# Kernel tuning notes

Measured on AMD Instinct MI355X. Metric: run time of the kernel, lower is better.

Reference implementation:

```python
import jax, jax.numpy as jnp
import numpy as np

EPS = 1e-7  # torchvision distance_box_iou_loss eps
BBOX_WEIGHT = 1.0


def _cxcywh_to_xyxy(b):
    cx, cy, w, h = b[..., 0], b[..., 1], b[..., 2], b[..., 3]
    return jnp.stack([cx - w / 2, cy - h / 2, cx + w / 2, cy + h / 2], axis=-1)


def _diou_loss(p, t):
    # p, t: broadcastable (..., 4) xyxy boxes -> (...) per-pair DIoU loss
    px1, py1, px2, py2 = p[..., 0], p[..., 1], p[..., 2], p[..., 3]
    tx1, ty1, tx2, ty2 = t[..., 0], t[..., 1], t[..., 2], t[..., 3]
    iw = jnp.clip(jnp.minimum(px2, tx2) - jnp.maximum(px1, tx1), 0.0)
    ih = jnp.clip(jnp.minimum(py2, ty2) - jnp.maximum(py1, ty1), 0.0)
    inter = iw * ih
    union = (px2 - px1) * (py2 - py1) + (tx2 - tx1) * (ty2 - ty1) - inter
    iou = inter / (union + EPS)
    cw = jnp.maximum(px2, tx2) - jnp.minimum(px1, tx1)
    ch = jnp.maximum(py2, ty2) - jnp.minimum(py1, ty1)
    diag2 = cw * cw + ch * ch + EPS
    dx = (px1 + px2) / 2 - (tx1 + tx2) / 2
    dy = (py1 + py2) / 2 - (ty1 + ty2) / 2
    return 1.0 - iou + (dx * dx + dy * dy) / diag2


def _smooth_l1_mean(p, t):
    # nn.SmoothL1Loss(reduction='none', beta=1.0) then .mean(-1)
    d = p - t
    ad = jnp.abs(d)
    return jnp.where(ad < 1.0, 0.5 * d * d, ad - 0.5).mean(-1)


def _pair_bbox_loss(p_xyxy, t_xyxy):
    # MyBBoxLoss with weight1 = weight2 = 1
    return _diou_loss(p_xyxy, t_xyxy) + _smooth_l1_mean(p_xyxy, t_xyxy)


def _hungarian_square(cost):
    # exact Hungarian (shortest augmenting path, e-maxx formulation), square n x n
    # returns col assignment per row; matches scipy.linear_sum_assignment optimum
    n = cost.shape[0]
    INF = np.inf
    u = np.zeros(n + 1)
    v = np.zeros(n + 1)
    p = np.zeros(n + 1, dtype=np.int64)  # p[j] = row matched to col j (1-based)
    for i in range(1, n + 1):
        p[0] = i
        j0 = 0
        minv = np.full(n + 1, INF)
        way = np.zeros(n + 1, dtype=np.int64)
        used = np.zeros(n + 1, dtype=bool)
        while True:
            used[j0] = True
            i0 = p[j0]
            cur = np.concatenate(([INF], cost[i0 - 1, :] - u[i0] - v[1:]))
            cur[used] = INF
            upd = cur < minv
            way[upd] = j0
            minv = np.where(upd, cur, minv)
            masked = np.where(used, INF, minv)
            j1 = int(np.argmin(masked))
            delta = masked[j1]
            u[p[used]] += delta
            v[used] -= delta
            minv[~used] -= delta
            j0 = j1
            if p[j0] == 0:
                break
        while j0 != 0:
            j1 = way[j0]
            p[j0] = p[j1]
            j0 = j1
    ans = np.zeros(n, dtype=np.int64)
    for j in range(1, n + 1):
        ans[p[j] - 1] = j - 1
    return ans


def _lsa(cost):
    # rectangular (N, M), N <= M: pad with constant rows (doesn't change optimum)
    N, M = cost.shape
    sq = np.zeros((M, M), dtype=np.float64)
    sq[:N] = cost
    return _hungarian_square(sq)[:N]


def compute_cost_and_assign(targ_cat, targ_bbox, pred_cat, pred_bbox):
    B, N = targ_cat.shape
    C = pred_cat.shape[2]
    # cat_cost[b,n,m] = -pred_cat[b,m,targ_cat[b,n]] via one-hot GEMM
    cat_cost = -jnp.einsum('bmc,bnc->bnm', pred_cat,
                           jax.nn.one_hot(targ_cat, C, dtype=pred_cat.dtype))
    t_xyxy = _cxcywh_to_xyxy(targ_bbox)  # (B,N,4)
    p_xyxy = _cxcywh_to_xyxy(pred_bbox)  # (B,M,4)
    bbox_cost = _pair_bbox_loss(p_xyxy[:, None, :, :], t_xyxy[:, :, None, :])  # (B,N,M)
    # faithful to source: multiply by (targ_cat == 0) mask
    bbox_cost = bbox_cost * (targ_cat == 0)[:, :, None].astype(bbox_cost.dtype)
    cost = cat_cost + BBOX_WEIGHT * bbox_cost
    cost_np = np.asarray(jax.device_get(cost), dtype=np.float64)
    assign = jnp.asarray(np.stack([_lsa(cost_np[b]) for b in range(B)]))  # (B,N)
    return assign


def setup_inputs() -> dict:
    key = jax.random.key(0)
    k1, k2, k3, k4 = jax.random.split(key, 4)
    B, N, M, C = 64, 100, 100, 92
    return {
        'targ_cat': jax.random.randint(k1, (B, N), 0, C),
        'targ_bbox': jax.random.uniform(k2, (B, N, 4), dtype=jnp.float32),
        'pred_cat': jax.random.normal(k3, (B, M, C), dtype=jnp.float32),
        'pred_bbox': jax.random.uniform(k4, (B, M, 4), dtype=jnp.float32),
    }


def reference(targ_cat, targ_bbox, pred_cat, pred_bbox):
    assign = compute_cost_and_assign(targ_cat, targ_bbox, pred_cat, pred_bbox)
    # gather matched predictions: (B,N,C) and (B,N,4)
    pc = jnp.take_along_axis(pred_cat, assign[:, :, None], axis=1)
    pb = jnp.take_along_axis(pred_bbox, assign[:, :, None], axis=1)
    # class loss: mean cross-entropy over all B*N slots
    logp = jax.nn.log_softmax(pc, axis=-1)
    loss_cat = -jnp.take_along_axis(logp, targ_cat[:, :, None], axis=2)[..., 0].mean()
    # bbox loss on matched pairs, masked to real objects (targ_cat != 0)
    lb = _pair_bbox_loss(_cxcywh_to_xyxy(pb), _cxcywh_to_xyxy(targ_bbox))  # (B,N)
    mask = targ_cat != 0
    loss_bbox = jnp.where(mask, lb, 0.0).sum() / mask.sum().astype(lb.dtype)
    loss = loss_cat + BBOX_WEIGHT * loss_bbox
    return loss, assign
```

## Files before the change

### kernel.cpp

```cpp
#include <hip/hip_runtime.h>
#include <hip/hip_bf16.h>
#include <math.h>

#define B_ 64
#define N_ 100
#define C_ 92


__device__ __forceinline__ void cxcywh_to_xyxy(const float q[4], float o[4]) {
#pragma clang fp contract(off)
  float cx = q[0], cy = q[1], w = q[2], h = q[3];
  o[0] = cx - w * 0.5f;
  o[1] = cy - h * 0.5f;
  o[2] = cx + w * 0.5f;
  o[3] = cy + h * 0.5f;
}

__device__ __forceinline__ float pair_bbox_loss(const float* p, const float* t) {
#pragma clang fp contract(off)
  const float EPS = 1e-7f;
  float px1 = p[0], py1 = p[1], px2 = p[2], py2 = p[3];
  float tx1 = t[0], ty1 = t[1], tx2 = t[2], ty2 = t[3];
  float iw = fminf(px2, tx2) - fmaxf(px1, tx1); iw = fmaxf(iw, 0.0f);
  float ih = fminf(py2, ty2) - fmaxf(py1, ty1); ih = fmaxf(ih, 0.0f);
  float inter = iw * ih;
  float uni = (px2 - px1) * (py2 - py1) + (tx2 - tx1) * (ty2 - ty1) - inter;
  float iou = inter / (uni + EPS);
  float cw = fmaxf(px2, tx2) - fminf(px1, tx1);
  float ch = fmaxf(py2, ty2) - fminf(py1, ty1);
  float diag2 = cw * cw + ch * ch + EPS;
  float dx = (px1 + px2) * 0.5f - (tx1 + tx2) * 0.5f;
  float dy = (py1 + py2) * 0.5f - (ty1 + ty2) * 0.5f;
  float diou = 1.0f - iou + (dx * dx + dy * dy) / diag2;
  float s = 0.0f;
  for (int k = 0; k < 4; ++k) {
    float d = p[k] - t[k];
    float ad = fabsf(d);
    s += (ad < 1.0f) ? 0.5f * d * d : ad - 0.5f;
  }
  return diou + s * 0.25f;
}

__device__ __forceinline__ int rdlane(int v, int srcLane) {
  return __builtin_amdgcn_readlane(v, srcLane);
}

template <int CTRL>
__device__ __forceinline__ double dminstep(double x) {
  int lo = __double2loint(x), hi = __double2hiint(x);
  int slo = __builtin_amdgcn_update_dpp(lo, lo, CTRL, 0xF, 0xF, false);
  int shi = __builtin_amdgcn_update_dpp(hi, hi, CTRL, 0xF, 0xF, false);
  return fmin(x, __hiloint2double(shi, slo));
}

__device__ __forceinline__ double read_u(double uA, double uB, int i0) {
  bool inA = (i0 <= 64);
  double src = inA ? uA : uB;
  int idx = inA ? (i0 - 1) : (i0 - 65);
  int lo = rdlane(__double2loint(src), idx);
  int hi = rdlane(__double2hiint(src), idx);
  return __hiloint2double(hi, lo);
}


__global__ __launch_bounds__(64) void hungarian_k(
    const int* __restrict__ targ_cat, const float* __restrict__ targ_bbox,
    const float* __restrict__ pred_cat, const float* __restrict__ pred_bbox,
    int* __restrict__ assign_ws, float* __restrict__ assign_out) {
  const int b = blockIdx.x;
  const int lane = threadIdx.x;

  __shared__ float costL[N_ * N_];
  __shared__ float tb[N_ * 4];
  __shared__ float pbx[N_ * 4];
  __shared__ int tcat[N_];

  for (int i = lane; i < N_; i += 64) {
    float q[4], o[4];
    q[0] = targ_bbox[(b * N_ + i) * 4 + 0];
    q[1] = targ_bbox[(b * N_ + i) * 4 + 1];
    q[2] = targ_bbox[(b * N_ + i) * 4 + 2];
    q[3] = targ_bbox[(b * N_ + i) * 4 + 3];
    cxcywh_to_xyxy(q, o);
    tb[i * 4 + 0] = o[0]; tb[i * 4 + 1] = o[1]; tb[i * 4 + 2] = o[2]; tb[i * 4 + 3] = o[3];
    q[0] = pred_bbox[(b * N_ + i) * 4 + 0];
    q[1] = pred_bbox[(b * N_ + i) * 4 + 1];
    q[2] = pred_bbox[(b * N_ + i) * 4 + 2];
    q[3] = pred_bbox[(b * N_ + i) * 4 + 3];
    cxcywh_to_xyxy(q, o);
    pbx[i * 4 + 0] = o[0]; pbx[i * 4 + 1] = o[1]; pbx[i * 4 + 2] = o[2]; pbx[i * 4 + 3] = o[3];
    tcat[i] = targ_cat[b * N_ + i];
  }
  __syncthreads();

  for (int e = lane; e < N_ * N_; e += 64) {
    int n = e / N_;
    int m = e - n * N_;
    int tc = tcat[n];
    float cc = -pred_cat[(b * N_ + m) * C_ + tc];
    float pl = pair_bbox_loss(&pbx[m * 4], &tb[n * 4]);
    costL[e] = cc + ((tc == 0) ? pl : 0.0f);
  }
  __syncthreads();

  const double INF = __builtin_huge_val();
  const int jA = lane + 1;
  const int jB = lane + 65;
  const bool hasB = (jB <= N_);

  double vA = 0.0, vB = 0.0;
  double uA = 0.0, uB = 0.0;
  int pA = 0, pB = 0;

  for (int i = 1; i <= N_; ++i) {
    double minvA = INF, minvB = INF;
    int wayA = 0, wayB = 0;
    bool usedA = false, usedB = false;
    bool fA = false, fB = false;
    int j0 = 0;
    int i0 = i;
    double ui0 = read_u(uA, uB, i0);
    float cA = costL[(i0 - 1) * N_ + (jA - 1)];
    float cB = 0.0f;
    if (hasB) cB = costL[(i0 - 1) * N_ + (jB - 1)];
    int it = 0;
    bool ok = true;

    while (true) {
      if (j0 == jA) usedA = true;
      if (j0 == jB) usedB = true;
      fA = fA || (i0 == jA);
      fB = fB || (i0 == jB);

      if (!usedA) {
        double cur = (double)cA - ui0 - vA;
        if (cur < minvA) { minvA = cur; wayA = j0; }
      }
      if (hasB && !usedB) {
        double cur = (double)cB - ui0 - vB;
        if (cur < minvB) { minvB = cur; wayB = j0; }
      }

      double cvA = usedA ? INF : minvA;
      double cvB = (hasB && !usedB) ? minvB : INF;
      double r = fmin(cvA, cvB);
      r = dminstep<0x111>(r);
      r = dminstep<0x112>(r);
      r = dminstep<0x114>(r);
      r = dminstep<0x118>(r);
      r = dminstep<0x142>(r);
      r = dminstep<0x143>(r);
      double delta = __hiloint2double(rdlane(__double2hiint(r), 63),
                                      rdlane(__double2loint(r), 63));
      if (delta == INF) { ok = false; break; }

      unsigned long long mA = __ballot(cvA == delta);
      int j1;
      if (mA) {
        j1 = __builtin_ctzll(mA) + 1;
      } else {
        unsigned long long mB = __ballot(cvB == delta);
        if (!mB) { ok = false; break; }
        j1 = __builtin_ctzll(mB) + 65;
      }

      int pj1 = (j1 <= 64) ? rdlane(pA, j1 - 1) : rdlane(pB, j1 - 65);
      int ni0 = (pj1 == 0) ? 1 : pj1;
      float nA = costL[(ni0 - 1) * N_ + (jA - 1)];
      float nB = 0.0f;
      if (hasB) nB = costL[(ni0 - 1) * N_ + (jB - 1)];
      double nui0 = read_u(uA, uB, ni0);

      if (fA) uA += delta;
      if (fB) uB += delta;
      if (usedA) { vA -= delta; } else { minvA -= delta; }
      if (hasB) {
        if (usedB) { vB -= delta; } else { minvB -= delta; }
      }

      j0 = j1;
      if (pj1 == 0) break;
      i0 = ni0; ui0 = nui0; cA = nA; cB = nB;
      if (++it > 2 * N_ + 8) { ok = false; break; }
    }

    if (ok) {
      int jj = j0;
      int hop = 0;
      while (jj != 0 && ++hop <= N_ + 2) {
        int jp = (jj <= 64) ? rdlane(wayA, jj - 1) : rdlane(wayB, jj - 65);
        int pv = (jp == 0) ? i
                           : ((jp <= 64) ? rdlane(pA, jp - 1) : rdlane(pB, jp - 65));
        if (jj <= 64) { if (lane == jj - 1) pA = pv; }
        else          { if (lane == jj - 65) pB = pv; }
        jj = jp;
      }
    }
  }

  {
    int row = pA - 1;
    if (row < 0) row = 0;
    if (row >= N_) row = N_ - 1;
    assign_ws[b * N_ + row] = jA - 1;
    assign_out[b * N_ + row] = (float)(jA - 1);
    if (hasB) {
      int r2 = pB - 1;
      if (r2 < 0) r2 = 0;
      if (r2 >= N_) r2 = N_ - 1;
      assign_ws[b * N_ + r2] = jB - 1;
      assign_out[b * N_ + r2] = (float)(jB - 1);
    }
  }
}


__global__ __launch_bounds__(256) void loss_rows_k(
    const int* __restrict__ targ_cat, const float* __restrict__ targ_bbox,
    const float* __restrict__ pred_cat, const float* __restrict__ pred_bbox,
    const int* __restrict__ assign,
    float* __restrict__ ce, float* __restrict__ lb, int* __restrict__ msk) {
  int t = blockIdx.x * blockDim.x + threadIdx.x;
  if (t >= B_ * N_) return;
  int b = t / N_;
  int m = assign[t];
  if (m < 0) m = 0;
  if (m >= N_) m = N_ - 1;
  int tc = targ_cat[t];

  const float* row = &pred_cat[(b * N_ + m) * C_];
  float mx = -INFINITY;
  for (int c = 0; c < C_; ++c) mx = fmaxf(mx, row[c]);
  float se = 0.0f;
  for (int c = 0; c < C_; ++c) se += expf(row[c] - mx);
  ce[t] = mx + logf(se) - row[tc];

  float q[4], po[4], to_[4];
  q[0] = pred_bbox[(b * N_ + m) * 4 + 0];
  q[1] = pred_bbox[(b * N_ + m) * 4 + 1];
  q[2] = pred_bbox[(b * N_ + m) * 4 + 2];
  q[3] = pred_bbox[(b * N_ + m) * 4 + 3];
  cxcywh_to_xyxy(q, po);
  q[0] = targ_bbox[t * 4 + 0];
  q[1] = targ_bbox[t * 4 + 1];
  q[2] = targ_bbox[t * 4 + 2];
  q[3] = targ_bbox[t * 4 + 3];
  cxcywh_to_xyxy(q, to_);
  float l = pair_bbox_loss(po, to_);
  bool mk = (tc != 0);
  lb[t] = mk ? l : 0.0f;
  msk[t] = mk ? 1 : 0;
}


__global__ __launch_bounds__(256) void finalize_k(
    const float* __restrict__ ce, const float* __restrict__ lb,
    const int* __restrict__ msk, float* __restrict__ out) {
  __shared__ double s1[256];
  __shared__ double s2[256];
  __shared__ int s3[256];
  int tid = threadIdx.x;
  double a = 0.0, c2 = 0.0;
  int c3 = 0;
  for (int t = tid; t < B_ * N_; t += 256) {
    a += (double)ce[t]; c2 += (double)lb[t]; c3 += msk[t];
  }
  s1[tid] = a; s2[tid] = c2; s3[tid] = c3;
  __syncthreads();
  for (int off = 128; off > 0; off >>= 1) {
    if (tid < off) {
      s1[tid] += s1[tid + off]; s2[tid] += s2[tid + off]; s3[tid] += s3[tid + off];
    }
    __syncthreads();
  }
  if (tid == 0) {
    double loss = s1[0] / (double)(B_ * N_) + s2[0] / (double)s3[0];
    out[0] = (float)loss;
  }
}

extern "C" void kernel_launch(void* const* d_in, const int* in_sizes, int n_in,
                              void* d_out, int out_size, void* d_ws, size_t ws_size,
                              hipStream_t stream) {
  const int* targ_cat = (const int*)d_in[0];
  const float* targ_bbox = (const float*)d_in[1];
  const float* pred_cat = (const float*)d_in[2];
  const float* pred_bbox = (const float*)d_in[3];
  float* out = (float*)d_out;

  char* ws = (char*)d_ws;
  int* assign_ws = (int*)(ws);
  float* ce = (float*)(ws + (32 << 10));
  float* lb = (float*)(ws + (64 << 10));
  int* msk = (int*)(ws + (96 << 10));

  hipLaunchKernelGGL(hungarian_k, dim3(B_), dim3(64), 0, stream,
                     targ_cat, targ_bbox, pred_cat, pred_bbox, assign_ws, out + 1);
  hipLaunchKernelGGL(loss_rows_k, dim3((B_ * N_ + 255) / 256), dim3(256), 0, stream,
                     targ_cat, targ_bbox, pred_cat, pred_bbox, assign_ws, ce, lb, msk);
  hipLaunchKernelGGL(finalize_k, dim3(1), dim3(256), 0, stream, ce, lb, msk, out);
}
```

Measured before the change: 597.6 us.

## Cache Hungarian cost columns in registers and vectorize softmax row loads

Each lane now preloads its cost-matrix column (two columns for lanes with B) into vector registers before the Hungarian loop. Per-step cost lookups become a register extract indexed by the wave-uniform row, replacing LDS reads. The two ballots are issued together instead of one conditionally, and the loss kernel loads each pred_cat row with float4 reads into a register array. This adds heavy register pressure (hence launch_bounds 64,1) and a select chain per extract, which may cause scratch spills or slow dynamic indexing.

```diff
diff --git a/kernel.cpp b/kernel.cpp
--- a/kernel.cpp
+++ b/kernel.cpp
@@ -5,6 +5,9 @@
 #define B_ 64
 #define N_ 100
 #define C_ 92
+
+typedef float f32x32 __attribute__((ext_vector_type(32)));
+typedef float f32x4  __attribute__((ext_vector_type(4)));
 
 
 __device__ __forceinline__ void cxcywh_to_xyxy(const float q[4], float o[4]) {
@@ -62,8 +65,21 @@
   return __hiloint2double(hi, lo);
 }
 
-
-__global__ __launch_bounds__(64) void hungarian_k(
+__device__ __forceinline__ float vext100(const f32x32& a0, const f32x32& a1,
+                                         const f32x32& a2, const f32x4& a3, int r) {
+  int off = r & 31;
+  int q = r >> 5;
+  float e0 = a0[off];
+  float e1 = a1[off];
+  float e2 = a2[off];
+  float e3 = a3[off & 3];
+  float x01 = (q & 1) ? e1 : e0;
+  float x23 = (q & 1) ? e3 : e2;
+  return (q & 2) ? x23 : x01;
+}
+
+
+__global__ __launch_bounds__(64, 1) void hungarian_k(
     const int* __restrict__ targ_cat, const float* __restrict__ targ_bbox,
     const float* __restrict__ pred_cat, const float* __restrict__ pred_bbox,
     int* __restrict__ assign_ws, float* __restrict__ assign_out) {
@@ -108,6 +124,27 @@
   const int jB = lane + 65;
   const bool hasB = (jB <= N_);
 
+  f32x32 a0, a1, a2; f32x4 a3;
+  f32x32 b0 = {}, b1 = {}, b2 = {}; f32x4 b3 = {};
+#pragma unroll
+  for (int k = 0; k < 32; ++k) {
+    a0[k] = costL[k * N_ + lane];
+    a1[k] = costL[(32 + k) * N_ + lane];
+    a2[k] = costL[(64 + k) * N_ + lane];
+  }
+#pragma unroll
+  for (int k = 0; k < 4; ++k) a3[k] = costL[(96 + k) * N_ + lane];
+  if (hasB) {
+#pragma unroll
+    for (int k = 0; k < 32; ++k) {
+      b0[k] = costL[k * N_ + lane + 64];
+      b1[k] = costL[(32 + k) * N_ + lane + 64];
+      b2[k] = costL[(64 + k) * N_ + lane + 64];
+    }
+#pragma unroll
+    for (int k = 0; k < 4; ++k) b3[k] = costL[(96 + k) * N_ + lane + 64];
+  }
+
   double vA = 0.0, vB = 0.0;
   double uA = 0.0, uB = 0.0;
   int pA = 0, pB = 0;
@@ -119,10 +156,6 @@
     bool fA = false, fB = false;
     int j0 = 0;
     int i0 = i;
-    double ui0 = read_u(uA, uB, i0);
-    float cA = costL[(i0 - 1) * N_ + (jA - 1)];
-    float cB = 0.0f;
-    if (hasB) cB = costL[(i0 - 1) * N_ + (jB - 1)];
     int it = 0;
     bool ok = true;
 
@@ -131,6 +164,11 @@
       if (j0 == jB) usedB = true;
       fA = fA || (i0 == jA);
       fB = fB || (i0 == jB);
+
+      int r = __builtin_amdgcn_readfirstlane(i0) - 1;
+      float cA = vext100(a0, a1, a2, a3, r);
+      float cB = vext100(b0, b1, b2, b3, r);
+      double ui0 = read_u(uA, uB, i0);
 
       if (!usedA) {
         double cur = (double)cA - ui0 - vA;
@@ -143,33 +181,24 @@
 
       double cvA = usedA ? INF : minvA;
       double cvB = (hasB && !usedB) ? minvB : INF;
-      double r = fmin(cvA, cvB);
-      r = dminstep<0x111>(r);
-      r = dminstep<0x112>(r);
-      r = dminstep<0x114>(r);
-      r = dminstep<0x118>(r);
-      r = dminstep<0x142>(r);
-      r = dminstep<0x143>(r);
-      double delta = __hiloint2double(rdlane(__double2hiint(r), 63),
-                                      rdlane(__double2loint(r), 63));
+      double rm = fmin(cvA, cvB);
+      rm = dminstep<0x111>(rm);
+      rm = dminstep<0x112>(rm);
+      rm = dminstep<0x114>(rm);
+      rm = dminstep<0x118>(rm);
+      rm = dminstep<0x142>(rm);
+      rm = dminstep<0x143>(rm);
+      double delta = __hiloint2double(rdlane(__double2hiint(rm), 63),
+                                      rdlane(__double2loint(rm), 63));
       if (delta == INF) { ok = false; break; }
 
       unsigned long long mA = __ballot(cvA == delta);
-      int j1;
-      if (mA) {
-        j1 = __builtin_ctzll(mA) + 1;
-      } else {
-        unsigned long long mB = __ballot(cvB == delta);
-        if (!mB) { ok = false; break; }
-        j1 = __builtin_ctzll(mB) + 65;
-      }
+      unsigned long long mB = __ballot(cvB == delta);
+      int j1 = mA ? (__builtin_ctzll(mA) + 1)
+                  : (mB ? (__builtin_ctzll(mB) + 65) : 0);
+      if (j1 == 0) { ok = false; break; }
 
       int pj1 = (j1 <= 64) ? rdlane(pA, j1 - 1) : rdlane(pB, j1 - 65);
-      int ni0 = (pj1 == 0) ? 1 : pj1;
-      float nA = costL[(ni0 - 1) * N_ + (jA - 1)];
-      float nB = 0.0f;
-      if (hasB) nB = costL[(ni0 - 1) * N_ + (jB - 1)];
-      double nui0 = read_u(uA, uB, ni0);
 
       if (fA) uA += delta;
       if (fB) uB += delta;
@@ -180,7 +209,7 @@
 
       j0 = j1;
       if (pj1 == 0) break;
-      i0 = ni0; ui0 = nui0; cA = nA; cB = nB;
+      i0 = pj1;
       if (++it > 2 * N_ + 8) { ok = false; break; }
     }
 
@@ -229,11 +258,21 @@
   int tc = targ_cat[t];
 
   const float* row = &pred_cat[(b * N_ + m) * C_];
+  float vals[C_];
+  const float4* row4 = (const float4*)row;
+#pragma unroll
+  for (int k = 0; k < C_ / 4; ++k) {
+    float4 w = row4[k];
+    vals[4 * k + 0] = w.x; vals[4 * k + 1] = w.y;
+    vals[4 * k + 2] = w.z; vals[4 * k + 3] = w.w;
+  }
   float mx = -INFINITY;
-  for (int c = 0; c < C_; ++c) mx = fmaxf(mx, row[c]);
+#pragma unroll
+  for (int c = 0; c < C_; ++c) mx = fmaxf(mx, vals[c]);
   float se = 0.0f;
-  for (int c = 0; c < C_; ++c) se += expf(row[c] - mx);
-  ce[t] = mx + logf(se) - row[tc];
+#pragma unroll
+  for (int c = 0; c < C_; ++c) se += expf(vals[c] - mx);
+  ce[t] = mx + logf(se) - vals[tc];
 
   float q[4], po[4], to_[4];
   q[0] = pred_bbox[(b * N_ + m) * 4 + 0];
```

Result: slower. 645.0 us (+7.9%).

## Use 32-bit key min-reduction for Hungarian argmin with exact-double fallback on ties

Applied to the files above, without the earlier changes.

Replaces the per-iteration double-precision DPP min reduction with a reduction over an order-preserving 32-bit key built from each value's high word, and falls back to the full double reduction only when more than one lane ties on that key. This halves the DPP and readlane work on the serial critical path of the augmenting-path loop. The cost matrix gets 64 padding entries so the B-column loads become unconditional. The softmax row in the loss kernel is loaded with float4 into registers, which raises register pressure and uses dynamic indexing for vals[tc].

```diff
diff --git a/kernel.cpp b/kernel.cpp
--- a/kernel.cpp
+++ b/kernel.cpp
@@ -53,6 +53,13 @@
   return fmin(x, __hiloint2double(shi, slo));
 }
 
+template <int CTRL>
+__device__ __forceinline__ unsigned uminstep(unsigned x) {
+  int s = __builtin_amdgcn_update_dpp((int)x, (int)x, CTRL, 0xF, 0xF, false);
+  unsigned su = (unsigned)s;
+  return x < su ? x : su;
+}
+
 __device__ __forceinline__ double read_u(double uA, double uB, int i0) {
   bool inA = (i0 <= 64);
   double src = inA ? uA : uB;
@@ -70,7 +77,7 @@
   const int b = blockIdx.x;
   const int lane = threadIdx.x;
 
-  __shared__ float costL[N_ * N_];
+  __shared__ float costL[N_ * N_ + 64];
   __shared__ float tb[N_ * 4];
   __shared__ float pbx[N_ * 4];
   __shared__ int tcat[N_];
@@ -91,6 +98,7 @@
     pbx[i * 4 + 0] = o[0]; pbx[i * 4 + 1] = o[1]; pbx[i * 4 + 2] = o[2]; pbx[i * 4 + 3] = o[3];
     tcat[i] = targ_cat[b * N_ + i];
   }
+  costL[N_ * N_ + lane] = 0.0f;
   __syncthreads();
 
   for (int e = lane; e < N_ * N_; e += 64) {
@@ -104,6 +112,7 @@
   __syncthreads();
 
   const double INF = __builtin_huge_val();
+  const unsigned INF_KEY = 0xFFF00000u;
   const int jA = lane + 1;
   const int jB = lane + 65;
   const bool hasB = (jB <= N_);
@@ -119,10 +128,10 @@
     bool fA = false, fB = false;
     int j0 = 0;
     int i0 = i;
+    const float* base0 = &costL[(i0 - 1) * N_ + lane];
+    float cA = base0[0];
+    float cB = base0[64];
     double ui0 = read_u(uA, uB, i0);
-    float cA = costL[(i0 - 1) * N_ + (jA - 1)];
-    float cB = 0.0f;
-    if (hasB) cB = costL[(i0 - 1) * N_ + (jB - 1)];
     int it = 0;
     bool ok = true;
 
@@ -143,44 +152,71 @@
 
       double cvA = usedA ? INF : minvA;
       double cvB = (hasB && !usedB) ? minvB : INF;
-      double r = fmin(cvA, cvB);
-      r = dminstep<0x111>(r);
-      r = dminstep<0x112>(r);
-      r = dminstep<0x114>(r);
-      r = dminstep<0x118>(r);
-      r = dminstep<0x142>(r);
-      r = dminstep<0x143>(r);
-      double delta = __hiloint2double(rdlane(__double2hiint(r), 63),
-                                      rdlane(__double2loint(r), 63));
-      if (delta == INF) { ok = false; break; }
-
-      unsigned long long mA = __ballot(cvA == delta);
+      double cv = fmin(cvA, cvB);
+
+      int hi = __double2hiint(cv);
+      unsigned key = (unsigned)hi ^ ((hi < 0) ? 0xFFFFFFFFu : 0x80000000u);
+      unsigned kr = key;
+      kr = uminstep<0x111>(kr);
+      kr = uminstep<0x112>(kr);
+      kr = uminstep<0x114>(kr);
+      kr = uminstep<0x118>(kr);
+      kr = uminstep<0x142>(kr);
+      kr = uminstep<0x143>(kr);
+      unsigned kmin = (unsigned)rdlane((int)kr, 63);
+      if (kmin == INF_KEY) { ok = false; break; }
+
+      unsigned long long tied = __ballot(key == kmin);
+      unsigned long long aWins = __ballot(cvA <= cvB);
       int j1;
-      if (mA) {
-        j1 = __builtin_ctzll(mA) + 1;
+      double delta;
+      if (__popcll(tied) == 1) {
+        int l = __builtin_ctzll(tied);
+        j1 = ((aWins >> l) & 1ull) ? (l + 1) : (l + 65);
+        int pj1x = (j1 <= 64) ? rdlane(pA, j1 - 1) : rdlane(pB, j1 - 65);
+        int ni0 = (pj1x == 0) ? 1 : pj1x;
+        const float* nb = &costL[(ni0 - 1) * N_ + lane];
+        float nA = nb[0];
+        float nB = nb[64];
+        double nui0 = read_u(uA, uB, ni0);
+        delta = __hiloint2double(rdlane(__double2hiint(cv), l),
+                                 rdlane(__double2loint(cv), l));
+        if (fA) uA += delta;
+        if (fB) uB += delta;
+        if (usedA) { vA -= delta; } else { minvA -= delta; }
+        if (hasB) { if (usedB) { vB -= delta; } else { minvB -= delta; } }
+        j0 = j1;
+        if (pj1x == 0) break;
+        i0 = ni0; ui0 = nui0; cA = nA; cB = nB;
       } else {
+        double rm = cv;
+        rm = dminstep<0x111>(rm);
+        rm = dminstep<0x112>(rm);
+        rm = dminstep<0x114>(rm);
+        rm = dminstep<0x118>(rm);
+        rm = dminstep<0x142>(rm);
+        rm = dminstep<0x143>(rm);
+        delta = __hiloint2double(rdlane(__double2hiint(rm), 63),
+                                 rdlane(__double2loint(rm), 63));
+        unsigned long long mA = __ballot(cvA == delta);
         unsigned long long mB = __ballot(cvB == delta);
-        if (!mB) { ok = false; break; }
-        j1 = __builtin_ctzll(mB) + 65;
+        j1 = mA ? (__builtin_ctzll(mA) + 1)
+                : (mB ? (__builtin_ctzll(mB) + 65) : 0);
+        if (j1 == 0) { ok = false; break; }
+        int pj1x = (j1 <= 64) ? rdlane(pA, j1 - 1) : rdlane(pB, j1 - 65);
+        int ni0 = (pj1x == 0) ? 1 : pj1x;
+        const float* nb = &costL[(ni0 - 1) * N_ + lane];
+        float nA = nb[0];
+        float nB = nb[64];
+        double nui0 = read_u(uA, uB, ni0);
+        if (fA) uA += delta;
+        if (fB) uB += delta;
+        if (usedA) { vA -= delta; } else { minvA -= delta; }
+        if (hasB) { if (usedB) { vB -= delta; } else { minvB -= delta; } }
+        j0 = j1;
+        if (pj1x == 0) break;
+        i0 = ni0; ui0 = nui0; cA = nA; cB = nB;
       }
-
-      int pj1 = (j1 <= 64) ? rdlane(pA, j1 - 1) : rdlane(pB, j1 - 65);
-      int ni0 = (pj1 == 0) ? 1 : pj1;
-      float nA = costL[(ni0 - 1) * N_ + (jA - 1)];
-      float nB = 0.0f;
-      if (hasB) nB = costL[(ni0 - 1) * N_ + (jB - 1)];
-      double nui0 = read_u(uA, uB, ni0);
-
-      if (fA) uA += delta;
-      if (fB) uB += delta;
-      if (usedA) { vA -= delta; } else { minvA -= delta; }
-      if (hasB) {
-        if (usedB) { vB -= delta; } else { minvB -= delta; }
-      }
-
-      j0 = j1;
-      if (pj1 == 0) break;
-      i0 = ni0; ui0 = nui0; cA = nA; cB = nB;
       if (++it > 2 * N_ + 8) { ok = false; break; }
     }
 
@@ -229,11 +265,21 @@
   int tc = targ_cat[t];
 
   const float* row = &pred_cat[(b * N_ + m) * C_];
+  float vals[C_];
+  const float4* row4 = (const float4*)row;
+#pragma unroll
+  for (int k = 0; k < C_ / 4; ++k) {
+    float4 w = row4[k];
+    vals[4 * k + 0] = w.x; vals[4 * k + 1] = w.y;
+    vals[4 * k + 2] = w.z; vals[4 * k + 3] = w.w;
+  }
   float mx = -INFINITY;
-  for (int c = 0; c < C_; ++c) mx = fmaxf(mx, row[c]);
+#pragma unroll
+  for (int c = 0; c < C_; ++c) mx = fmaxf(mx, vals[c]);
   float se = 0.0f;
-  for (int c = 0; c < C_; ++c) se += expf(row[c] - mx);
-  ce[t] = mx + logf(se) - row[tc];
+#pragma unroll
+  for (int c = 0; c < C_; ++c) se += expf(vals[c] - mx);
+  ce[t] = mx + logf(se) - vals[tc];
 
   float q[4], po[4], to_[4];
   q[0] = pred_bbox[(b * N_ + m) * 4 + 0];
```

After: 714.8 us. 19.6% more time.
